# Performance work log

Hardware: AMD Instinct MI355X
Metric: run time of the kernel (lower is better)

## Reference

```python
import jax, jax.numpy as jnp
import numpy as np
from jax import lax

CODEBOOK_DIM = 32
SCALE_SCHEDULE = [1, 2, 4, 8, 16, 32, 64, 128, 256, 512, 1024, 2048, 4096, 8192]
INV_TEMP = 100.0
COMMIT_W = 0.2
ENTROPY_W = 0.1
EPS_NORM = 1e-12
EPS_LOG = 1e-8


def setup_inputs() -> dict:
    key = jax.random.key(0)
    B, T, C = 32, 8192, CODEBOOK_DIM
    f_BTC = jax.random.normal(key, (B, T, C), dtype=jnp.float32)
    return {"f_BTC": f_BTC}


def _area_down(x, pt):
    # torch F.interpolate mode='area' on divisible sizes == average pooling
    B, T, C = x.shape
    if pt == T:
        return x
    return x.reshape(B, pt, T // pt, C).mean(axis=2)


def _linear_up(x, out_size):
    # torch F.interpolate mode='linear', align_corners=False
    B, in_size, C = x.shape
    if out_size == in_size:
        return x
    scale = in_size / out_size
    pos = (jnp.arange(out_size, dtype=jnp.float32) + 0.5) * scale - 0.5
    pos = jnp.clip(pos, 0.0, in_size - 1)
    lo = jnp.floor(pos).astype(jnp.int32)
    hi = jnp.minimum(lo + 1, in_size - 1)
    w = (pos - lo.astype(jnp.float32))[None, :, None]
    return x[:, lo] * (1.0 - w) + x[:, hi] * w


def _bsq_level(z):
    # normalize
    norm = jnp.sqrt(jnp.sum(z * z, axis=-1, keepdims=True))
    z = z / jnp.maximum(norm, EPS_NORM)
    q_scale = 1.0 / (CODEBOOK_DIM ** 0.5)
    zhat = jnp.where(z > 0, q_scale, -q_scale).astype(z.dtype)
    quant = z + lax.stop_gradient(zhat - z)  # STE
    # soft entropy loss
    p = jax.nn.sigmoid(-4.0 * z / (CODEBOOK_DIM ** 0.5) * INV_TEMP)
    ent = lambda c: -(c * jnp.log(c + EPS_LOG))
    per_sample = (ent(p) + ent(1.0 - p)).sum(axis=-1).mean()
    avg_p = p.mean(axis=(0, 1))  # [C]
    cb_ent = (ent(avg_p) + ent(1.0 - avg_p)).sum()
    entropy_penalty = (per_sample - cb_ent) / INV_TEMP
    commit = jnp.mean(((lax.stop_gradient(quant) - z) ** 2).sum(axis=-1))
    aux = entropy_penalty * ENTROPY_W + commit * COMMIT_W
    bits = (quant > 0).astype(jnp.int32)
    return quant, bits, aux


def reference(f_BTC):
    B, T, C = f_BTC.shape
    quantized_out = jnp.zeros_like(f_BTC)
    residual = f_BTC
    all_losses, all_bits = [], []
    for pt in SCALE_SCHEDULE:
        r = _area_down(residual, pt)
        quant, bits, loss = _bsq_level(r)
        q_up = _linear_up(quant, T)
        residual = residual - lax.stop_gradient(q_up)
        quantized_out = quantized_out + q_up
        all_bits.append(bits)
        all_losses.append(loss)
    return quantized_out, jnp.concatenate(all_bits, axis=1), jnp.stack(all_losses, axis=-1)
```

## Files before the change

kernel.cpp:

```cpp
#include <hip/hip_runtime.h>

#define B_DIM 32
#define T_DIM 8192
#define C_DIM 32
#define N_ELEM (B_DIM * T_DIM * C_DIM)
#define SUM_PT 16383
#define BITS_ELEM (B_DIM * SUM_PT * C_DIM)
#define NLEVEL 14
#define PARTW 2048
#define QSCALE 0.17677669529663687f
#define ALPHA  70.710678118654755f

#define OWN 128
#define HALO 16
#define MAXL (OWN + 2 * HALO)

__device__ __forceinline__ float entf(float x) { return -(x * __logf(x + 1e-8f)); }
__device__ __forceinline__ float qval(float bit) { return bit * (2.0f * QSCALE) - QSCALE; }

__device__ __forceinline__ float interp_pk(const unsigned int* __restrict__ pkbase,
                                           int ptj, float tpos, int c) {
    const float a = (float)ptj * (1.0f / (float)T_DIM);
    float pos = (tpos + 0.5f) * a - 0.5f;
    pos = fminf(fmaxf(pos, 0.0f), (float)(ptj - 1));
    const int lo = (int)pos;
    const int hi = min(lo + 1, ptj - 1);
    const float w = pos - (float)lo;
    const float b0 = (float)((pkbase[lo] >> c) & 1u);
    const float b1 = (float)((pkbase[hi] >> c) & 1u);
    return ((b0 * (1.0f - w) + b1 * w) * 2.0f - 1.0f) * QSCALE;
}

__device__ __forceinline__ float corr_mid_local(const unsigned int* __restrict__ bl,
                                                int ptk, int row, int c, int p0, int pN) {
    const float a = (float)ptk * (1.0f / (float)T_DIM);
    float pos = (float)(2 * row + 1) * a - 0.5f;
    pos = fminf(fmaxf(pos, 0.0f), (float)(ptk - 1));
    const int lo = (int)pos;
    const int hi = min(lo + 1, ptk - 1);
    const float w = pos - (float)lo;
    const int lol = min(max(lo - p0, 0), pN - 1);
    const int hil = min(max(hi - p0, 0), pN - 1);
    const float b0 = (float)((bl[lol] >> c) & 1u);
    const float b1 = (float)((bl[hil] >> c) & 1u);
    return ((b0 * (1.0f - w) + b1 * w) * 2.0f - 1.0f) * QSCALE;
}

__device__ float pooled_up_sum64(const float* base, int ptj, int m) {
    const int W = 64;
    const float a = (float)ptj * (1.0f / (float)T_DIM);
    const float p0 = ((float)(m * W) + 0.5f) * a - 0.5f;
    const float pmax = (float)(ptj - 1);
    float sum = 0.0f;
    int iL = 0;
    if (p0 < 0.0f) { iL = (int)ceilf(-p0 / a); if (iL > W) iL = W; }
    int iH = W - 1;
    if (p0 + (float)(W - 1) * a > pmax) {
        iH = (int)floorf((pmax - p0) / a);
        if (iH > W - 1) iH = W - 1;
        if (iH < -1) iH = -1;
    }
    if (iL > 0) sum += (float)iL * qval(base[0]);
    if (iH < W - 1) sum += (float)(W - 1 - iH) * qval(base[(size_t)(ptj - 1) * C_DIM]);
    if (iH >= iL) {
        const float pL = p0 + (float)iL * a;
        int l0 = (int)pL;
        if (l0 > ptj - 1) l0 = ptj - 1;
        const int is = (int)ceilf(((float)(l0 + 1) - p0) / a);
        const int endA = min(is - 1, iH);
        if (endA >= iL) {
            const int nA = endA - iL + 1;
            const float sI = 0.5f * (float)(iL + endA) * (float)nA;
            const float SA = (float)nA * (p0 - (float)l0) + a * sI;
            const float q0 = qval(base[(size_t)l0 * C_DIM]);
            const float q1 = qval(base[(size_t)min(l0 + 1, ptj - 1) * C_DIM]);
            sum += (float)nA * q0 + SA * (q1 - q0);
        }
        const int begB = max(is, iL);
        if (begB <= iH) {
            const int nB = iH - begB + 1;
            const float sI = 0.5f * (float)(begB + iH) * (float)nB;
            const float SB = (float)nB * (p0 - (float)(l0 + 1)) + a * sI;
            const float q1 = qval(base[(size_t)min(l0 + 1, ptj - 1) * C_DIM]);
            const float q2 = qval(base[(size_t)min(l0 + 2, ptj - 1) * C_DIM]);
            sum += (float)nB * q1 + SB * (q2 - q1);
        }
    }
    return sum;
}

template <int NT>
__device__ __forceinline__ void write_partials(float eAcc, float cAcc, float pAcc,
                                               float* partial, int level, int col) {
    __shared__ float sP[NT];
    __shared__ float sEC[NT / 16];
    __syncthreads();
    const int grp = threadIdx.x >> 5, c = threadIdx.x & 31;
    float eg = eAcc, cg = cAcc;
#pragma unroll
    for (int m = 16; m >= 1; m >>= 1) { eg += __shfl_xor(eg, m, 32); cg += __shfl_xor(cg, m, 32); }
    if (c == 0) { sEC[grp * 2] = eg; sEC[grp * 2 + 1] = cg; }
    sP[threadIdx.x] = pAcc;
    __syncthreads();
    float* base = partial + (size_t)level * 34 * PARTW;
    if (threadIdx.x < 32) {
        float ps = 0.f;
#pragma unroll
        for (int r = 0; r < NT / 32; ++r) ps += sP[threadIdx.x + r * 32];
        base[(size_t)(2 + threadIdx.x) * PARTW + col] = ps;
    }
    if (threadIdx.x == 0) {
        float se = 0.f, sc = 0.f;
#pragma unroll
        for (int g = 0; g < NT / 32; ++g) { se += sEC[2 * g]; sc += sEC[2 * g + 1]; }
        base[0 * PARTW + col] = se;
        base[(size_t)1 * PARTW + col] = sc;
    }
}

__device__ __forceinline__ float bsq_eval(float v, float& bit, float& pA, float& eA, float& cA) {
    float sq = v * v;
#pragma unroll
    for (int m = 16; m >= 1; m >>= 1) sq += __shfl_xor(sq, m, 32);
    const float z = v / fmaxf(sqrtf(sq), 1e-12f);
    bit = (z > 0.f) ? 1.0f : 0.0f;
    const float zh = (z > 0.f) ? QSCALE : -QSCALE;
    const float d = zh - z;
    cA += d * d;
    const float p = 1.0f / (1.0f + __expf(ALPHA * z));
    pA += p;
    eA += entf(p) + entf(1.0f - p);
    return zh;
}

__global__ void init_kernel(const float* __restrict__ f, float* __restrict__ F128) {
    const int b = blockIdx.x >> 7, m = blockIdx.x & 127;
    const int c = threadIdx.x & 31, grp = threadIdx.x >> 5;
    const float* fb = f + ((size_t)b * T_DIM + m * 64 + grp * 8) * C_DIM + c;
    float s = 0.f;
#pragma unroll
    for (int i = 0; i < 8; ++i) s += fb[i * C_DIM];
    __shared__ float red[8][32];
    red[grp][c] = s;
    __syncthreads();
    if (grp == 0) {
        float t = red[0][c] + red[1][c] + red[2][c] + red[3][c]
                + red[4][c] + red[5][c] + red[6][c] + red[7][c];
        F128[((size_t)b * 128 + m) * C_DIM + c] = t * (1.0f / 64.0f);
    }
}

__global__ __launch_bounds__(1024) void fused_small_kernel(const float* __restrict__ F128,
                                                           float* __restrict__ bits,
                                                           unsigned int* __restrict__ pkG,
                                                           float* __restrict__ partial) {
    const int b = blockIdx.x;
    __shared__ float P[128 * 32];
    __shared__ float qh[127 * 32];
    const int c = threadIdx.x & 31, grp = threadIdx.x >> 5;
    for (int i = threadIdx.x; i < 128 * 32; i += 1024) P[i] = F128[(size_t)b * 128 * 32 + i];
    __syncthreads();
    for (int k = 0; k < 8; ++k) {
        const int pt = 1 << k, W2 = 128 >> k;
        float pAcc = 0.f, eAcc = 0.f, cAcc = 0.f;
        for (int o = grp; o < pt; o += 32) {
            float v = 0.f;
            for (int i = 0; i < W2; ++i) v += P[(o * W2 + i) * 32 + c];
            v *= (1.0f / (float)W2);
            float bit;
            bsq_eval(v, bit, pAcc, eAcc, cAcc);
            bits[((size_t)b * SUM_PT + (pt - 1) + o) * C_DIM + c] = bit;
            const unsigned long long bal = __ballot(bit > 0.5f);
            if (c == 0)
                pkG[(size_t)b * 8192 + (pt - 1) + o] =
                    (threadIdx.x & 32) ? (unsigned)(bal >> 32) : (unsigned)bal;
            if (k < 7) qh[((pt - 1) + o) * 32 + c] = bit;
        }
        write_partials<1024>(eAcc, cAcc, pAcc, partial, k, b);
        if (k < 7) {
            __syncthreads();
            for (int m = grp; m < 128; m += 32)
                P[m * 32 + c] -= pooled_up_sum64(&qh[(pt - 1) * 32 + c], 1 << k, m) * (1.0f / 64.0f);
            __syncthreads();
        }
    }
}

__global__ __launch_bounds__(256) void chunk_kernel(const float* __restrict__ f,
                                                    float* __restrict__ bits,
                                                    unsigned int* __restrict__ pkG,
                                                    float* __restrict__ partial) {
    const int b = blockIdx.x >> 5;
    const int chunk = blockIdx.x & 31;
    const int r0 = chunk * OWN, r1 = r0 + OWN;
    const int L0 = max(0, r0 - HALO);
    const int L1 = min(4096, r1 + HALO);
    const int nL = L1 - L0;
    const int nSeg = nL >> 4;
    __shared__ float Rl[MAXL * 32];
    __shared__ unsigned int bitsL[310];
    __shared__ unsigned int pk07[255];
    __shared__ float segA[10][32], segB[10][32];
    const int c = threadIdx.x & 31, grp = threadIdx.x >> 5;

    const float* fb = f + ((size_t)b * T_DIM + (size_t)L0 * 2) * C_DIM;
    for (int i = threadIdx.x; i < nL * 8; i += 256) {
        const int row = i >> 3, c4 = i & 7;
        const float4 v0 = *(const float4*)(fb + (size_t)(2 * row) * 32 + c4 * 4);
        const float4 v1 = *(const float4*)(fb + (size_t)(2 * row + 1) * 32 + c4 * 4);
        float4 o;
        o.x = 0.5f * (v0.x + v1.x); o.y = 0.5f * (v0.y + v1.y);
        o.z = 0.5f * (v0.z + v1.z); o.w = 0.5f * (v0.w + v1.w);
        *(float4*)(Rl + row * 32 + c4 * 4) = o;
    }
    for (int i = threadIdx.x; i < 255; i += 256) pk07[i] = pkG[(size_t)b * 8192 + i];
    __syncthreads();

    for (int w = threadIdx.x; w < nSeg * 32; w += 256) {
        const int s = w >> 5, cc = w & 31;
        const int rg = L0 + s * 16;
        float c0 = 0.f, c1 = 0.f;
#pragma unroll
        for (int j = 0; j < 8; ++j) {
            const int ptj = 1 << j;
            c0 += interp_pk(pk07 + (ptj - 1), ptj, (float)(2 * rg) + 0.5f, cc);
            c1 += interp_pk(pk07 + (ptj - 1), ptj, (float)(2 * rg + 2) + 0.5f, cc);
        }
        segA[s][cc] = c0;
        segB[s][cc] = c1 - c0;
    }
    __syncthreads();
    for (int rl = grp; rl < nL; rl += 8) {
        const int s = rl >> 4;
        Rl[rl * 32 + c] -= fmaf((float)(rl & 15), segB[s][c], segA[s][c]);
    }
    __syncthreads();

    const int offs[5] = {0, 10, 30, 70, 150};
    for (int k = 8; k <= 12; ++k) {
        const int F = 4096 >> k;
        const int ptk = 1 << k;
        const int p0 = L0 / F, pN = nL / F;
        const int own0 = r0 / F, own1 = r1 / F;
        const int off = offs[k - 8];
        float pAcc = 0.f, eAcc = 0.f, cAcc = 0.f;
        for (int pl = grp; pl < pN; pl += 8) {
            float v = 0.f;
            for (int r = 0; r < F; ++r) v += Rl[(pl * F + r) * 32 + c];
            v *= (1.0f / (float)F);
            float sq = v * v;
#pragma unroll
            for (int m = 16; m >= 1; m >>= 1) sq += __shfl_xor(sq, m, 32);
            const float z = v / fmaxf(sqrtf(sq), 1e-12f);
            const unsigned long long bal = __ballot(z > 0.f);
            const unsigned int word = (threadIdx.x & 32) ? (unsigned)(bal >> 32) : (unsigned)bal;
            if (c == 0) bitsL[off + pl] = word;
            const int mg = p0 + pl;
            if (mg >= own0 && mg < own1) {
                bits[((size_t)b * SUM_PT + (ptk - 1) + mg) * C_DIM + c] = (z > 0.f) ? 1.f : 0.f;
                if (c == 0) pkG[(size_t)b * 8192 + (ptk - 1) + mg] = word;
                const float zh = (z > 0.f) ? QSCALE : -QSCALE;
                const float d = zh - z;
                cAcc += d * d;
                const float p = 1.0f / (1.0f + __expf(ALPHA * z));
                pAcc += p;
                eAcc += entf(p) + entf(1.0f - p);
            }
        }
        write_partials<256>(eAcc, cAcc, pAcc, partial, k, blockIdx.x);
        __syncthreads();
        if (k < 12) {
            for (int rl = grp; rl < nL; rl += 8)
                Rl[rl * 32 + c] -= corr_mid_local(bitsL + off, ptk, L0 + rl, c, p0, pN);
            __syncthreads();
        }
    }
}

__global__ __launch_bounds__(256) void final_kernel(const float* __restrict__ f,
                                                    float* __restrict__ outQ,
                                                    float* __restrict__ bits,
                                                    const unsigned int* __restrict__ pkG,
                                                    float* __restrict__ partial) {
    const int b = blockIdx.x >> 5;
    const int sub = blockIdx.x & 31;
    const int t0 = sub * 256;
    __shared__ unsigned int pkW[764];
    __shared__ float segA[16][32], segB[16][32];
    const int c = threadIdx.x & 31, grp = threadIdx.x >> 5;
    const unsigned int* pgb = pkG + (size_t)b * 8192;
    for (int i = threadIdx.x; i < 511; i += 256) pkW[i] = pgb[i];
    int woff[4], wbase[4];
    int o = 511;
#pragma unroll
    for (int j = 9; j <= 12; ++j) {
        const int ptj = 1 << j;
        const int w0 = max(0, ((t0 * ptj) >> 13) - 1);
        const int w1 = min(ptj - 1, (((t0 + 256) * ptj) >> 13) + 1);
        const int cnt = w1 - w0 + 1;
        for (int i = threadIdx.x; i < cnt; i += 256) pkW[o + i] = pgb[(ptj - 1) + w0 + i];
        woff[j - 9] = o;
        wbase[j - 9] = w0;
        o += cnt;
    }
    __syncthreads();
    for (int w = threadIdx.x; w < 512; w += 256) {
        const int s = w >> 5, cc = w & 31;
        const int tA = t0 + s * 16;
        float c0 = 0.f, c1 = 0.f;
#pragma unroll
        for (int j = 0; j <= 8; ++j) {
            const int ptj = 1 << j;
            c0 += interp_pk(pkW + (ptj - 1), ptj, (float)tA, cc);
            c1 += interp_pk(pkW + (ptj - 1), ptj, (float)(tA + 1), cc);
        }
        segA[s][cc] = c0;
        segB[s][cc] = c1 - c0;
    }
    __syncthreads();
    float pAcc = 0.f, eAcc = 0.f, cAcc = 0.f;
    for (int tt = grp; tt < 256; tt += 8) {
        const int t = t0 + tt;
        float up = fmaf((float)(tt & 15), segB[tt >> 4][c], segA[tt >> 4][c]);
#pragma unroll
        for (int j = 9; j <= 12; ++j) {
            const int ptj = 1 << j;
            const float a = (float)ptj * (1.0f / (float)T_DIM);
            float pos = ((float)t + 0.5f) * a - 0.5f;
            pos = fminf(fmaxf(pos, 0.0f), (float)(ptj - 1));
            const int lo = (int)pos;
            const int hi = min(lo + 1, ptj - 1);
            const float w = pos - (float)lo;
            const unsigned int* base = pkW + (woff[j - 9] - wbase[j - 9]);
            const float b0 = (float)((base[lo] >> c) & 1u);
            const float b1 = (float)((base[hi] >> c) & 1u);
            up += ((b0 * (1.0f - w) + b1 * w) * 2.0f - 1.0f) * QSCALE;
        }
        const size_t idx = ((size_t)b * T_DIM + t) * C_DIM + c;
        const float v = f[idx] - up;
        float bit;
        const float zh = bsq_eval(v, bit, pAcc, eAcc, cAcc);
        bits[((size_t)b * SUM_PT + (T_DIM - 1) + t) * C_DIM + c] = bit;
        outQ[idx] = up + zh;
    }
    write_partials<256>(eAcc, cAcc, pAcc, partial, 13, blockIdx.x);
}

__global__ void reduce_partials(const float* __restrict__ partial, float* __restrict__ acc) {
    const int level = blockIdx.x / 34;
    const int comp = blockIdx.x % 34;
    const int nblk = (level < 8) ? 32 : 1024;
    const float* s = partial + ((size_t)level * 34 + comp) * PARTW;
    float v = 0.f;
    for (int i = threadIdx.x; i < nblk; i += 64) v += s[i];
#pragma unroll
    for (int m = 32; m >= 1; m >>= 1) v += __shfl_xor(v, m, 64);
    if (threadIdx.x == 0) acc[level * 64 + comp] = v;
}

__global__ void finalize_kernel(const float* __restrict__ acc, float* __restrict__ outL) {
    const int k = threadIdx.x >> 5;
    const int c = threadIdx.x & 31;
    if (k >= NLEVEL) return;
    const float cnt = (float)(B_DIM << k);
    const float avg_p = acc[k * 64 + 2 + c] / cnt;
    float ec = entf(avg_p) + entf(1.0f - avg_p);
#pragma unroll
    for (int m = 16; m >= 1; m >>= 1) ec += __shfl_xor(ec, m, 32);
    if (c == 0) {
        const float per_sample = acc[k * 64 + 0] / cnt;
        const float commit = acc[k * 64 + 1] / cnt;
        const float pen = (per_sample - ec) * (1.0f / 100.0f);
        outL[k] = pen * 0.1f + commit * 0.2f;
    }
}

extern "C" void kernel_launch(void* const* d_in, const int* in_sizes, int n_in,
                              void* d_out, int out_size, void* d_ws, size_t ws_size,
                              hipStream_t stream) {
    (void)in_sizes; (void)n_in; (void)out_size; (void)ws_size;
    const float* f = (const float*)d_in[0];
    float* outQ = (float*)d_out;
    float* outBits = outQ + N_ELEM;
    float* outL = outBits + BITS_ELEM;

    float* partial = (float*)d_ws;
    float* acc = partial + (size_t)NLEVEL * 34 * PARTW;
    float* F128 = acc + NLEVEL * 64;
    unsigned int* pkG = (unsigned int*)(F128 + (size_t)B_DIM * 128 * C_DIM);

    init_kernel<<<B_DIM * 128, 256, 0, stream>>>(f, F128);
    fused_small_kernel<<<B_DIM, 1024, 0, stream>>>(F128, outBits, pkG, partial);
    chunk_kernel<<<B_DIM * 32, 256, 0, stream>>>(f, outBits, pkG, partial);
    final_kernel<<<B_DIM * 32, 256, 0, stream>>>(f, outQ, outBits, pkG, partial);
    reduce_partials<<<NLEVEL * 34, 64, 0, stream>>>(partial, acc);
    finalize_kernel<<<1, 512, 0, stream>>>(acc, outL);
}
```

Measured before the change: 172.2 us.

## Fuse chunk and final kernels using halo-local bit pyramid; merge reductions

Merges the mid-level (8–12) chunk kernel and the final-level kernel into one kernel. Each block now owns half as many rows and keeps its level 8–12 bit words in shared memory, so the final level no longer goes through the global packed-bit buffer or needs a separate launch. The two reduction kernels are also merged into a single-block reduce+finalize, and the per-level loops are templated so they can unroll. The cost is more halo recomputation with smaller chunks, a serial single-block reduction over 2048 partials per component, and less parallelism in that last step.

Measured after the change: 229.9 us. 33.5% more time.

```diff
diff --git a/kernel.cpp b/kernel.cpp
--- a/kernel.cpp
+++ b/kernel.cpp
@@ -11,7 +11,7 @@
 #define QSCALE 0.17677669529663687f
 #define ALPHA  70.710678118654755f
 
-#define OWN 128
+#define OWN 64
 #define HALO 16
 #define MAXL (OWN + 2 * HALO)
 
@@ -31,13 +31,28 @@
     return ((b0 * (1.0f - w) + b1 * w) * 2.0f - 1.0f) * QSCALE;
 }
 
+template <int PTJ>
+__device__ __forceinline__ float interp_loc(const unsigned int* __restrict__ bl,
+                                            int p0, float tpos, int c) {
+    const float a = (float)PTJ * (1.0f / (float)T_DIM);
+    float pos = (tpos + 0.5f) * a - 0.5f;
+    pos = fminf(fmaxf(pos, 0.0f), (float)(PTJ - 1));
+    const int lo = (int)pos;
+    const int hi = min(lo + 1, PTJ - 1);
+    const float w = pos - (float)lo;
+    const float b0 = (float)((bl[lo - p0] >> c) & 1u);
+    const float b1 = (float)((bl[hi - p0] >> c) & 1u);
+    return ((b0 * (1.0f - w) + b1 * w) * 2.0f - 1.0f) * QSCALE;
+}
+
+template <int PTK>
 __device__ __forceinline__ float corr_mid_local(const unsigned int* __restrict__ bl,
-                                                int ptk, int row, int c, int p0, int pN) {
-    const float a = (float)ptk * (1.0f / (float)T_DIM);
+                                                int row, int c, int p0, int pN) {
+    const float a = (float)PTK * (1.0f / (float)T_DIM);
     float pos = (float)(2 * row + 1) * a - 0.5f;
-    pos = fminf(fmaxf(pos, 0.0f), (float)(ptk - 1));
+    pos = fminf(fmaxf(pos, 0.0f), (float)(PTK - 1));
     const int lo = (int)pos;
-    const int hi = min(lo + 1, ptk - 1);
+    const int hi = min(lo + 1, PTK - 1);
     const float w = pos - (float)lo;
     const int lol = min(max(lo - p0, 0), pN - 1);
     const int hil = min(max(hi - p0, 0), pN - 1);
@@ -172,7 +187,7 @@
             bits[((size_t)b * SUM_PT + (pt - 1) + o) * C_DIM + c] = bit;
             const unsigned long long bal = __ballot(bit > 0.5f);
             if (c == 0)
-                pkG[(size_t)b * 8192 + (pt - 1) + o] =
+                pkG[(size_t)b * 256 + (pt - 1) + o] =
                     (threadIdx.x & 32) ? (unsigned)(bal >> 32) : (unsigned)bal;
             if (k < 7) qh[((pt - 1) + o) * 32 + c] = bit;
         }
@@ -186,21 +201,65 @@
     }
 }
 
-__global__ __launch_bounds__(256) void chunk_kernel(const float* __restrict__ f,
-                                                    float* __restrict__ bits,
-                                                    unsigned int* __restrict__ pkG,
-                                                    float* __restrict__ partial) {
-    const int b = blockIdx.x >> 5;
-    const int chunk = blockIdx.x & 31;
+template <int K, int OFF>
+__device__ __forceinline__ void cf_level(float* Rl, unsigned int* bitsPyr,
+                                         float* __restrict__ bits,
+                                         float* __restrict__ partial, int b,
+                                         int L0, int nL, int r0, int r1,
+                                         int c, int grp) {
+    constexpr int F = 4096 >> K;
+    constexpr int ptk = 1 << K;
+    const int p0 = L0 / F, pN = nL / F;
+    const int own0 = r0 / F, own1 = r1 / F;
+    unsigned int* bl = bitsPyr + OFF;
+    float pAcc = 0.f, eAcc = 0.f, cAcc = 0.f;
+    for (int pl = grp; pl < pN; pl += 8) {
+        float v = 0.f;
+#pragma unroll
+        for (int r = 0; r < F; ++r) v += Rl[(pl * F + r) * 32 + c];
+        v *= (1.0f / (float)F);
+        float sq = v * v;
+#pragma unroll
+        for (int m = 16; m >= 1; m >>= 1) sq += __shfl_xor(sq, m, 32);
+        const float z = v / fmaxf(sqrtf(sq), 1e-12f);
+        const unsigned long long bal = __ballot(z > 0.f);
+        const unsigned int word = (threadIdx.x & 32) ? (unsigned)(bal >> 32) : (unsigned)bal;
+        if (c == 0) bl[pl] = word;
+        const int mg = p0 + pl;
+        if (mg >= own0 && mg < own1) {
+            bits[((size_t)b * SUM_PT + (ptk - 1) + mg) * C_DIM + c] = (z > 0.f) ? 1.f : 0.f;
+            const float zh = (z > 0.f) ? QSCALE : -QSCALE;
+            const float d = zh - z;
+            cAcc += d * d;
+            const float p = 1.0f / (1.0f + __expf(ALPHA * z));
+            pAcc += p;
+            eAcc += entf(p) + entf(1.0f - p);
+        }
+    }
+    write_partials<256>(eAcc, cAcc, pAcc, partial, K, blockIdx.x);
+    if (K < 12) {
+        for (int rl = grp; rl < nL; rl += 8)
+            Rl[rl * 32 + c] -= corr_mid_local<ptk>(bl, L0 + rl, c, p0, pN);
+        __syncthreads();
+    }
+}
+
+__global__ __launch_bounds__(256) void chunk_final_kernel(const float* __restrict__ f,
+                                                          float* __restrict__ outQ,
+                                                          float* __restrict__ bits,
+                                                          const unsigned int* __restrict__ pkG,
+                                                          float* __restrict__ partial) {
+    const int b = blockIdx.x >> 6;
+    const int chunk = blockIdx.x & 63;
     const int r0 = chunk * OWN, r1 = r0 + OWN;
     const int L0 = max(0, r0 - HALO);
     const int L1 = min(4096, r1 + HALO);
     const int nL = L1 - L0;
     const int nSeg = nL >> 4;
     __shared__ float Rl[MAXL * 32];
-    __shared__ unsigned int bitsL[310];
+    __shared__ unsigned int bitsPyr[186];
     __shared__ unsigned int pk07[255];
-    __shared__ float segA[10][32], segB[10][32];
+    __shared__ float segA[8][32], segB[8][32];
     const int c = threadIdx.x & 31, grp = threadIdx.x >> 5;
 
     const float* fb = f + ((size_t)b * T_DIM + (size_t)L0 * 2) * C_DIM;
@@ -213,7 +272,7 @@
         o.z = 0.5f * (v0.z + v1.z); o.w = 0.5f * (v0.w + v1.w);
         *(float4*)(Rl + row * 32 + c4 * 4) = o;
     }
-    for (int i = threadIdx.x; i < 255; i += 256) pk07[i] = pkG[(size_t)b * 8192 + i];
+    for (int i = threadIdx.x; i < 255; i += 256) pk07[i] = pkG[(size_t)b * 256 + i];
     __syncthreads();
 
     for (int w = threadIdx.x; w < nSeg * 32; w += 256) {
@@ -236,106 +295,39 @@
     }
     __syncthreads();
 
-    const int offs[5] = {0, 10, 30, 70, 150};
-    for (int k = 8; k <= 12; ++k) {
-        const int F = 4096 >> k;
-        const int ptk = 1 << k;
-        const int p0 = L0 / F, pN = nL / F;
-        const int own0 = r0 / F, own1 = r1 / F;
-        const int off = offs[k - 8];
-        float pAcc = 0.f, eAcc = 0.f, cAcc = 0.f;
-        for (int pl = grp; pl < pN; pl += 8) {
-            float v = 0.f;
-            for (int r = 0; r < F; ++r) v += Rl[(pl * F + r) * 32 + c];
-            v *= (1.0f / (float)F);
-            float sq = v * v;
-#pragma unroll
-            for (int m = 16; m >= 1; m >>= 1) sq += __shfl_xor(sq, m, 32);
-            const float z = v / fmaxf(sqrtf(sq), 1e-12f);
-            const unsigned long long bal = __ballot(z > 0.f);
-            const unsigned int word = (threadIdx.x & 32) ? (unsigned)(bal >> 32) : (unsigned)bal;
-            if (c == 0) bitsL[off + pl] = word;
-            const int mg = p0 + pl;
-            if (mg >= own0 && mg < own1) {
-                bits[((size_t)b * SUM_PT + (ptk - 1) + mg) * C_DIM + c] = (z > 0.f) ? 1.f : 0.f;
-                if (c == 0) pkG[(size_t)b * 8192 + (ptk - 1) + mg] = word;
-                const float zh = (z > 0.f) ? QSCALE : -QSCALE;
-                const float d = zh - z;
-                cAcc += d * d;
-                const float p = 1.0f / (1.0f + __expf(ALPHA * z));
-                pAcc += p;
-                eAcc += entf(p) + entf(1.0f - p);
-            }
-        }
-        write_partials<256>(eAcc, cAcc, pAcc, partial, k, blockIdx.x);
-        __syncthreads();
-        if (k < 12) {
-            for (int rl = grp; rl < nL; rl += 8)
-                Rl[rl * 32 + c] -= corr_mid_local(bitsL + off, ptk, L0 + rl, c, p0, pN);
-            __syncthreads();
-        }
-    }
-}
-
-__global__ __launch_bounds__(256) void final_kernel(const float* __restrict__ f,
-                                                    float* __restrict__ outQ,
-                                                    float* __restrict__ bits,
-                                                    const unsigned int* __restrict__ pkG,
-                                                    float* __restrict__ partial) {
-    const int b = blockIdx.x >> 5;
-    const int sub = blockIdx.x & 31;
-    const int t0 = sub * 256;
-    __shared__ unsigned int pkW[764];
-    __shared__ float segA[16][32], segB[16][32];
-    const int c = threadIdx.x & 31, grp = threadIdx.x >> 5;
-    const unsigned int* pgb = pkG + (size_t)b * 8192;
-    for (int i = threadIdx.x; i < 511; i += 256) pkW[i] = pgb[i];
-    int woff[4], wbase[4];
-    int o = 511;
-#pragma unroll
-    for (int j = 9; j <= 12; ++j) {
-        const int ptj = 1 << j;
-        const int w0 = max(0, ((t0 * ptj) >> 13) - 1);
-        const int w1 = min(ptj - 1, (((t0 + 256) * ptj) >> 13) + 1);
-        const int cnt = w1 - w0 + 1;
-        for (int i = threadIdx.x; i < cnt; i += 256) pkW[o + i] = pgb[(ptj - 1) + w0 + i];
-        woff[j - 9] = o;
-        wbase[j - 9] = w0;
-        o += cnt;
-    }
-    __syncthreads();
-    for (int w = threadIdx.x; w < 512; w += 256) {
+    cf_level<8, 0>(Rl, bitsPyr, bits, partial, b, L0, nL, r0, r1, c, grp);
+    cf_level<9, 6>(Rl, bitsPyr, bits, partial, b, L0, nL, r0, r1, c, grp);
+    cf_level<10, 18>(Rl, bitsPyr, bits, partial, b, L0, nL, r0, r1, c, grp);
+    cf_level<11, 42>(Rl, bitsPyr, bits, partial, b, L0, nL, r0, r1, c, grp);
+    cf_level<12, 90>(Rl, bitsPyr, bits, partial, b, L0, nL, r0, r1, c, grp);
+
+    __syncthreads();
+    const int t0 = 2 * r0;
+    const int p8 = L0 / 16, p9 = L0 / 8, p10 = L0 / 4, p11 = L0 / 2, p12 = L0;
+    for (int w = threadIdx.x; w < 8 * 32; w += 256) {
         const int s = w >> 5, cc = w & 31;
         const int tA = t0 + s * 16;
         float c0 = 0.f, c1 = 0.f;
 #pragma unroll
-        for (int j = 0; j <= 8; ++j) {
+        for (int j = 0; j < 8; ++j) {
             const int ptj = 1 << j;
-            c0 += interp_pk(pkW + (ptj - 1), ptj, (float)tA, cc);
-            c1 += interp_pk(pkW + (ptj - 1), ptj, (float)(tA + 1), cc);
-        }
+            c0 += interp_pk(pk07 + (ptj - 1), ptj, (float)tA, cc);
+            c1 += interp_pk(pk07 + (ptj - 1), ptj, (float)(tA + 1), cc);
+        }
+        c0 += interp_loc<256>(bitsPyr + 0, p8, (float)tA, cc);
+        c1 += interp_loc<256>(bitsPyr + 0, p8, (float)(tA + 1), cc);
         segA[s][cc] = c0;
         segB[s][cc] = c1 - c0;
     }
     __syncthreads();
     float pAcc = 0.f, eAcc = 0.f, cAcc = 0.f;
-    for (int tt = grp; tt < 256; tt += 8) {
+    for (int tt = grp; tt < 2 * OWN; tt += 8) {
         const int t = t0 + tt;
         float up = fmaf((float)(tt & 15), segB[tt >> 4][c], segA[tt >> 4][c]);
-#pragma unroll
-        for (int j = 9; j <= 12; ++j) {
-            const int ptj = 1 << j;
-            const float a = (float)ptj * (1.0f / (float)T_DIM);
-            float pos = ((float)t + 0.5f) * a - 0.5f;
-            pos = fminf(fmaxf(pos, 0.0f), (float)(ptj - 1));
-            const int lo = (int)pos;
-            const int hi = min(lo + 1, ptj - 1);
-            const float w = pos - (float)lo;
-            const unsigned int* base = pkW + (woff[j - 9] - wbase[j - 9]);
-            const float b0 = (float)((base[lo] >> c) & 1u);
-            const float b1 = (float)((base[hi] >> c) & 1u);
-            up += ((b0 * (1.0f - w) + b1 * w) * 2.0f - 1.0f) * QSCALE;
-        }
+        up += interp_loc<512>(bitsPyr + 6, p9, (float)t, c);
+        up += interp_loc<1024>(bitsPyr + 18, p10, (float)t, c);
+        up += interp_loc<2048>(bitsPyr + 42, p11, (float)t, c);
+        up += interp_loc<4096>(bitsPyr + 90, p12, (float)t, c);
         const size_t idx = ((size_t)b * T_DIM + t) * C_DIM + c;
         const float v = f[idx] - up;
         float bit;
@@ -346,32 +338,34 @@
     write_partials<256>(eAcc, cAcc, pAcc, partial, 13, blockIdx.x);
 }
 
-__global__ void reduce_partials(const float* __restrict__ partial, float* __restrict__ acc) {
-    const int level = blockIdx.x / 34;
-    const int comp = blockIdx.x % 34;
-    const int nblk = (level < 8) ? 32 : 1024;
-    const float* s = partial + ((size_t)level * 34 + comp) * PARTW;
-    float v = 0.f;
-    for (int i = threadIdx.x; i < nblk; i += 64) v += s[i];
-#pragma unroll
-    for (int m = 32; m >= 1; m >>= 1) v += __shfl_xor(v, m, 64);
-    if (threadIdx.x == 0) acc[level * 64 + comp] = v;
-}
-
-__global__ void finalize_kernel(const float* __restrict__ acc, float* __restrict__ outL) {
-    const int k = threadIdx.x >> 5;
-    const int c = threadIdx.x & 31;
-    if (k >= NLEVEL) return;
-    const float cnt = (float)(B_DIM << k);
-    const float avg_p = acc[k * 64 + 2 + c] / cnt;
-    float ec = entf(avg_p) + entf(1.0f - avg_p);
-#pragma unroll
-    for (int m = 16; m >= 1; m >>= 1) ec += __shfl_xor(ec, m, 32);
-    if (c == 0) {
-        const float per_sample = acc[k * 64 + 0] / cnt;
-        const float commit = acc[k * 64 + 1] / cnt;
-        const float pen = (per_sample - ec) * (1.0f / 100.0f);
-        outL[k] = pen * 0.1f + commit * 0.2f;
+__global__ __launch_bounds__(1024) void reduce_finalize(const float* __restrict__ partial,
+                                                        float* __restrict__ outL) {
+    __shared__ float accS[NLEVEL * 34];
+    const int tid = threadIdx.x;
+    if (tid < NLEVEL * 34) {
+        const int level = tid / 34, comp = tid % 34;
+        const int nblk = (level < 8) ? 32 : 2048;
+        const float* s = partial + ((size_t)level * 34 + comp) * PARTW;
+        float v0 = 0.f, v1 = 0.f, v2 = 0.f, v3 = 0.f;
+        for (int i = 0; i < nblk; i += 4) {
+            v0 += s[i]; v1 += s[i + 1]; v2 += s[i + 2]; v3 += s[i + 3];
+        }
+        accS[tid] = (v0 + v1) + (v2 + v3);
+    }
+    __syncthreads();
+    const int k = tid >> 5, c = tid & 31;
+    if (k < NLEVEL) {
+        const float cnt = (float)(B_DIM << k);
+        const float avg_p = accS[k * 34 + 2 + c] / cnt;
+        float ec = entf(avg_p) + entf(1.0f - avg_p);
+#pragma unroll
+        for (int m = 16; m >= 1; m >>= 1) ec += __shfl_xor(ec, m, 32);
+        if (c == 0) {
+            const float per_sample = accS[k * 34 + 0] / cnt;
+            const float commit = accS[k * 34 + 1] / cnt;
+            const float pen = (per_sample - ec) * (1.0f / 100.0f);
+            outL[k] = pen * 0.1f + commit * 0.2f;
+        }
     }
 }
 
@@ -391,8 +385,6 @@
 
     init_kernel<<<B_DIM * 128, 256, 0, stream>>>(f, F128);
     fused_small_kernel<<<B_DIM, 1024, 0, stream>>>(F128, outBits, pkG, partial);
-    chunk_kernel<<<B_DIM * 32, 256, 0, stream>>>(f, outBits, pkG, partial);
-    final_kernel<<<B_DIM * 32, 256, 0, stream>>>(f, outQ, outBits, pkG, partial);
-    reduce_partials<<<NLEVEL * 34, 64, 0, stream>>>(partial, acc);
-    finalize_kernel<<<1, 512, 0, stream>>>(acc, outL);
-}
+    chunk_final_kernel<<<B_DIM * 64, 256, 0, stream>>>(f, outQ, outBits, pkG, partial);
+    reduce_finalize<<<1, 1024, 0, stream>>>(partial, outL);
+}
```
